# Kernel optimization log

Hardware: AMD Instinct MI355X
Metric: run time of the kernel (lower is better)

## Reference

```python
import math
import jax, jax.numpy as jnp
import numpy as np

NUM_RFS = 8192
DIM = 4096

# Elementwise coefficient functions (Performer softmax-kernel convention):
#   a_fun(t) = t (per-feature gaussian rescale), A_fun(t) = 1 (amplitude)
def _ab(xis):
    return xis

def _AB(xis):
    return jnp.ones_like(xis)

def input_to_rfs(xw, xis, gs, num_rfs):
    # xw: [dim], xis: [num_rfs], gs: [num_rfs, dim]
    ab = _ab(xis)                      # [num_rfs]
    AB = _AB(xis)                      # [num_rfs]
    # renorm_gs = ab[:,None]*gs ; dot = renorm_gs @ xw == ab * (gs @ xw)
    dot = ab * (gs @ xw)               # [num_rfs]
    corr = 0.5 * jnp.sum(xw * xw) * ab * ab
    return (1.0 / math.sqrt(num_rfs)) * AB * jnp.exp(dot - corr)


def setup_inputs() -> dict:
    key = jax.random.key(0)
    k1, k2, k3, k4, k5 = jax.random.split(key, 5)
    x = jax.random.normal(k1, (DIM,), dtype=jnp.float32)
    w = jax.random.normal(k2, (DIM,), dtype=jnp.float32)
    xis = jax.random.normal(k3, (NUM_RFS,), dtype=jnp.float32)
    # original uses torch.rand (uniform) for gs; materialize both draws
    gs_x = jax.random.uniform(k4, (NUM_RFS, DIM), dtype=jnp.float32)
    gs_w = jax.random.uniform(k5, (NUM_RFS, DIM), dtype=jnp.float32)
    return {"x": x, "w": w, "xis": xis, "gs_x": gs_x, "gs_w": gs_w}


def reference(x, w, xis, gs_x, gs_w):
    weights = input_to_rfs(w, xis, gs_w, NUM_RFS)   # [num_rfs] (init-time param)
    xb = input_to_rfs(x, xis, gs_x, NUM_RFS)        # [num_rfs]
    return xb @ weights                              # scalar
```

## Files before the change

### kernel.cpp

```cpp
#include <hip/hip_runtime.h>
#include <math.h>

#define DIM 4096
#define NRF 8192
#define NBLK 1024
#define TPB  512
#define NV4  (DIM / 4)
#define ROWS_PER_BLOCK 8

typedef float f32x4 __attribute__((ext_vector_type(4)));

__global__ __launch_bounds__(TPB, 4) void k_main(const f32x4* __restrict__ gsx,
                                                 const f32x4* __restrict__ gsw,
                                                 const float* __restrict__ xis,
                                                 const f32x4* __restrict__ x4,
                                                 const f32x4* __restrict__ w4,
                                                 float* __restrict__ out) {
    __shared__ f32x4 lx[NV4];
    __shared__ f32x4 lw[NV4];
    __shared__ float ssq_s[8];
    __shared__ float wsum[8];

    int t = threadIdx.x;
    int lane = t & 63;
    int wid  = t >> 6;

    f32x4 a0 = x4[t], a1 = x4[t + TPB];
    f32x4 b0 = w4[t], b1 = w4[t + TPB];
    lx[t] = a0; lx[t + TPB] = a1;
    lw[t] = b0; lw[t + TPB] = b1;

    float ssq = a0.x*a0.x + a0.y*a0.y + a0.z*a0.z + a0.w*a0.w
              + a1.x*a1.x + a1.y*a1.y + a1.z*a1.z + a1.w*a1.w
              + b0.x*b0.x + b0.y*b0.y + b0.z*b0.z + b0.w*b0.w
              + b1.x*b1.x + b1.y*b1.y + b1.z*b1.z + b1.w*b1.w;
    #pragma unroll
    for (int off = 32; off >= 1; off >>= 1) ssq += __shfl_xor(ssq, off);
    if (lane == 0) ssq_s[wid] = ssq;
    __syncthreads();
    float sxw = ssq_s[0] + ssq_s[1] + ssq_s[2] + ssq_s[3]
              + ssq_s[4] + ssq_s[5] + ssq_s[6] + ssq_s[7];

    int row = blockIdx.x * ROWS_PER_BLOCK + wid;
    const f32x4* __restrict__ rx = gsx + (size_t)row * NV4;
    const f32x4* __restrict__ rw = gsw + (size_t)row * NV4;

    float dx0 = 0.f, dx1 = 0.f, dw0 = 0.f, dw1 = 0.f;
    #pragma unroll
    for (int k = 0; k < NV4 / 64; k += 2) {
        f32x4 a = rx[k * 64 + lane];
        f32x4 b = lx[k * 64 + lane];
        dx0 += a.x*b.x + a.y*b.y + a.z*b.z + a.w*b.w;
        f32x4 c = rx[(k + 1) * 64 + lane];
        f32x4 d = lx[(k + 1) * 64 + lane];
        dx1 += c.x*d.x + c.y*d.y + c.z*d.z + c.w*d.w;
        f32x4 e = rw[k * 64 + lane];
        f32x4 f = lw[k * 64 + lane];
        dw0 += e.x*f.x + e.y*f.y + e.z*f.z + e.w*f.w;
        f32x4 g = rw[(k + 1) * 64 + lane];
        f32x4 h = lw[(k + 1) * 64 + lane];
        dw1 += g.x*h.x + g.y*h.y + g.z*h.z + g.w*h.w;
    }
    float s = (dx0 + dx1) + (dw0 + dw1);
    #pragma unroll
    for (int off = 32; off >= 1; off >>= 1) s += __shfl_xor(s, off);

    if (lane == 0) {
        float xi = xis[row];
        float e  = xi * s - 0.5f * xi * xi * sxw;
        wsum[wid] = expf(e);
    }
    __syncthreads();
    if (t == 0) {
        float bsum = (wsum[0] + wsum[1] + wsum[2] + wsum[3]
                    + wsum[4] + wsum[5] + wsum[6] + wsum[7]) * (1.0f / (float)NRF);
        atomicAdd(out, bsum);
    }
}

extern "C" void kernel_launch(void* const* d_in, const int* in_sizes, int n_in,
                              void* d_out, int out_size, void* d_ws, size_t ws_size,
                              hipStream_t stream) {
    const float* x    = (const float*)d_in[0];
    const float* w    = (const float*)d_in[1];
    const float* xis  = (const float*)d_in[2];
    const f32x4* gsx  = (const f32x4*)d_in[3];
    const f32x4* gsw  = (const f32x4*)d_in[4];
    float* out = (float*)d_out;

    hipMemsetAsync(out, 0, sizeof(float), stream);
    k_main<<<NBLK, TPB, 0, stream>>>(gsx, gsw, xis,
                                     (const f32x4*)x, (const f32x4*)w, out);
}
```

Before: 50.32 us.

## Drop LDS staging and atomics; write per-row partials and reduce in second kernel

```diff
diff --git a/kernel.cpp b/kernel.cpp
--- a/kernel.cpp
+++ b/kernel.cpp
@@ -3,79 +3,77 @@
 
 #define DIM 4096
 #define NRF 8192
-#define NBLK 1024
-#define TPB  512
 #define NV4  (DIM / 4)
-#define ROWS_PER_BLOCK 8
+#define TPB  256
+#define NBLK (NRF / 4)
 
 typedef float f32x4 __attribute__((ext_vector_type(4)));
 
-__global__ __launch_bounds__(TPB, 4) void k_main(const f32x4* __restrict__ gsx,
+__global__ __launch_bounds__(TPB, 8) void k_main(const f32x4* __restrict__ gsx,
                                                  const f32x4* __restrict__ gsw,
                                                  const float* __restrict__ xis,
                                                  const f32x4* __restrict__ x4,
                                                  const f32x4* __restrict__ w4,
-                                                 float* __restrict__ out) {
-    __shared__ f32x4 lx[NV4];
-    __shared__ f32x4 lw[NV4];
-    __shared__ float ssq_s[8];
-    __shared__ float wsum[8];
-
-    int t = threadIdx.x;
+                                                 float* __restrict__ partials) {
+    int t    = threadIdx.x;
     int lane = t & 63;
     int wid  = t >> 6;
 
-    f32x4 a0 = x4[t], a1 = x4[t + TPB];
-    f32x4 b0 = w4[t], b1 = w4[t + TPB];
-    lx[t] = a0; lx[t + TPB] = a1;
-    lw[t] = b0; lw[t + TPB] = b1;
-
-    float ssq = a0.x*a0.x + a0.y*a0.y + a0.z*a0.z + a0.w*a0.w
-              + a1.x*a1.x + a1.y*a1.y + a1.z*a1.z + a1.w*a1.w
-              + b0.x*b0.x + b0.y*b0.y + b0.z*b0.z + b0.w*b0.w
-              + b1.x*b1.x + b1.y*b1.y + b1.z*b1.z + b1.w*b1.w;
-    #pragma unroll
-    for (int off = 32; off >= 1; off >>= 1) ssq += __shfl_xor(ssq, off);
-    if (lane == 0) ssq_s[wid] = ssq;
-    __syncthreads();
-    float sxw = ssq_s[0] + ssq_s[1] + ssq_s[2] + ssq_s[3]
-              + ssq_s[4] + ssq_s[5] + ssq_s[6] + ssq_s[7];
-
-    int row = blockIdx.x * ROWS_PER_BLOCK + wid;
+    int row = blockIdx.x * 4 + wid;
     const f32x4* __restrict__ rx = gsx + (size_t)row * NV4;
     const f32x4* __restrict__ rw = gsw + (size_t)row * NV4;
 
     float dx0 = 0.f, dx1 = 0.f, dw0 = 0.f, dw1 = 0.f;
+    float sq0 = 0.f, sq1 = 0.f;
     #pragma unroll
     for (int k = 0; k < NV4 / 64; k += 2) {
         f32x4 a = rx[k * 64 + lane];
-        f32x4 b = lx[k * 64 + lane];
+        f32x4 b = x4[k * 64 + lane];
         dx0 += a.x*b.x + a.y*b.y + a.z*b.z + a.w*b.w;
+        sq0 += b.x*b.x + b.y*b.y + b.z*b.z + b.w*b.w;
         f32x4 c = rx[(k + 1) * 64 + lane];
-        f32x4 d = lx[(k + 1) * 64 + lane];
+        f32x4 d = x4[(k + 1) * 64 + lane];
         dx1 += c.x*d.x + c.y*d.y + c.z*d.z + c.w*d.w;
+        sq1 += d.x*d.x + d.y*d.y + d.z*d.z + d.w*d.w;
         f32x4 e = rw[k * 64 + lane];
-        f32x4 f = lw[k * 64 + lane];
+        f32x4 f = w4[k * 64 + lane];
         dw0 += e.x*f.x + e.y*f.y + e.z*f.z + e.w*f.w;
+        sq0 += f.x*f.x + f.y*f.y + f.z*f.z + f.w*f.w;
         f32x4 g = rw[(k + 1) * 64 + lane];
-        f32x4 h = lw[(k + 1) * 64 + lane];
+        f32x4 h = w4[(k + 1) * 64 + lane];
         dw1 += g.x*h.x + g.y*h.y + g.z*h.z + g.w*h.w;
+        sq1 += h.x*h.x + h.y*h.y + h.z*h.z + h.w*h.w;
     }
     float s = (dx0 + dx1) + (dw0 + dw1);
+    float q = sq0 + sq1;
     #pragma unroll
-    for (int off = 32; off >= 1; off >>= 1) s += __shfl_xor(s, off);
+    for (int off = 32; off >= 1; off >>= 1) {
+        s += __shfl_xor(s, off);
+        q += __shfl_xor(q, off);
+    }
 
     if (lane == 0) {
         float xi = xis[row];
-        float e  = xi * s - 0.5f * xi * xi * sxw;
-        wsum[wid] = expf(e);
+        float e  = xi * s - 0.5f * xi * xi * q;
+        partials[row] = expf(e);
     }
+}
+
+__global__ __launch_bounds__(256) void k_reduce(const f32x4* __restrict__ partials,
+                                                float* __restrict__ out) {
+    int t = threadIdx.x;
+    double a = 0.0;
+    #pragma unroll
+    for (int i = 0; i < (NRF / 4) / 256; ++i) {
+        f32x4 v = partials[t + i * 256];
+        a += (double)v.x + (double)v.y + (double)v.z + (double)v.w;
+    }
+    #pragma unroll
+    for (int off = 32; off >= 1; off >>= 1) a += __shfl_xor(a, off);
+    __shared__ double s[4];
+    if ((t & 63) == 0) s[t >> 6] = a;
     __syncthreads();
-    if (t == 0) {
-        float bsum = (wsum[0] + wsum[1] + wsum[2] + wsum[3]
-                    + wsum[4] + wsum[5] + wsum[6] + wsum[7]) * (1.0f / (float)NRF);
-        atomicAdd(out, bsum);
-    }
+    if (t == 0) out[0] = (float)((s[0] + s[1] + s[2] + s[3]) * (1.0 / (double)NRF));
 }
 
 extern "C" void kernel_launch(void* const* d_in, const int* in_sizes, int n_in,
@@ -88,7 +86,9 @@
     const f32x4* gsw  = (const f32x4*)d_in[4];
     float* out = (float*)d_out;
 
-    hipMemsetAsync(out, 0, sizeof(float), stream);
+    float* partials = (float*)d_ws;
+
     k_main<<<NBLK, TPB, 0, stream>>>(gsx, gsw, xis,
-                                     (const f32x4*)x, (const f32x4*)w, out);
+                                     (const f32x4*)x, (const f32x4*)w, partials);
+    k_reduce<<<1, 256, 0, stream>>>((const f32x4*)partials, out);
 }
```

Result: slower. 142.8 us (+183.9%).
